# Optimization experiments

Hardware: AMD Instinct MI355X
Metric: run time of the kernel (lower is better)

The kernel has to match this reference:

```python
import jax, jax.numpy as jnp
import numpy as np

SEG_LENS = (2048, 4096, 8192)
DIL_RATES = (1, 2, 4)
DIM = 1024
HEADS = 16
HEAD_DIM = DIM // HEADS
BATCH = 1
SEQ = sum(SEG_LENS)


def _hilbert_perm(L):
    """Permutation ordering the first L row-major cells of a 2^k x 2^k grid by Hilbert distance."""
    n = 1
    while n * n < L:
        n *= 2
    idx = np.arange(n * n, dtype=np.int64)
    x = idx % n
    y = idx // n
    d = np.zeros(n * n, dtype=np.int64)
    s = n // 2
    while s > 0:
        rx = ((x & s) > 0).astype(np.int64)
        ry = ((y & s) > 0).astype(np.int64)
        d += s * s * ((3 * rx) ^ ry)
        swap = ry == 0
        flip = swap & (rx == 1)
        x = np.where(flip, s - 1 - x, x)
        y = np.where(flip, s - 1 - y, y)
        x, y = np.where(swap, y, x), np.where(swap, x, y)
        s //= 2
    return np.argsort(d[:L], kind='stable')


def _segment_attn(x_seg, wqkv, bqkv, wo, bo, rate, use_hilbert=True):
    """HilbertAttentionCore: hilbert reorder -> QKV -> dilated attention -> out proj -> inverse reorder.
    x_seg: [B, L, D] -> [B, L, D]
    """
    B, L, D = x_seg.shape
    hd = D // HEADS
    perm_np = _hilbert_perm(L)
    perm = jnp.asarray(perm_np)
    inv = jnp.asarray(np.argsort(perm_np))
    xh = x_seg[:, perm] if use_hilbert else x_seg
    qkv = xh @ wqkv + bqkv                      # [B, L, 3D]
    q, k, v = jnp.split(qkv, 3, axis=-1)
    q = q.reshape(B, L, HEADS, hd)
    k = k.reshape(B, L, HEADS, hd)
    v = v.reshape(B, L, HEADS, hd)
    Lr = L // rate
    offs = jnp.arange(HEADS) % rate             # per-head dilation offset
    hidx = jnp.arange(HEADS)

    def dilate(t):
        # position i = off + rate*j  <->  reshape(L//rate, rate)[j, off]
        tr = t.reshape(B, Lr, rate, HEADS, hd)
        return tr[:, :, offs, hidx, :]          # [B, Lr, H, hd]

    qd, kd, vd = dilate(q), dilate(k), dilate(v)
    scale = 1.0 / np.sqrt(hd).astype(np.float32)
    scores = jnp.einsum('bihd,bjhd->bhij', qd, kd) * scale
    probs = jax.nn.softmax(scores, axis=-1)
    od = jnp.einsum('bhij,bjhd->bihd', probs, vd)  # [B, Lr, H, hd]
    # scatter each head's dilated subsequence back; uncovered (head,pos) stay zero
    outr = jnp.zeros((B, Lr, rate, HEADS, hd), x_seg.dtype)
    outr = outr.at[:, :, offs, hidx, :].set(od)
    out = outr.reshape(B, L, HEADS * hd) @ wo + bo
    return out[:, inv] if use_hilbert else out


def setup_inputs() -> dict:
    key = jax.random.key(0)
    ks = jax.random.split(key, 16)
    inp = {
        'q': jax.random.normal(ks[0], (BATCH, SEQ, HEADS, HEAD_DIM), jnp.float32),
        'k': jax.random.normal(ks[1], (BATCH, SEQ, HEADS, HEAD_DIM), jnp.float32),
        'v': jax.random.normal(ks[2], (BATCH, SEQ, HEADS, HEAD_DIM), jnp.float32),
    }
    for i in range(3):
        inp[f'wqkv_{i}'] = jax.random.normal(ks[3 + 4 * i], (DIM, 3 * DIM), jnp.float32) * 0.02
        inp[f'bqkv_{i}'] = jnp.zeros((3 * DIM,), jnp.float32)
        inp[f'wo_{i}'] = jax.random.normal(ks[4 + 4 * i], (DIM, DIM), jnp.float32) * 0.02
        inp[f'bo_{i}'] = jnp.zeros((DIM,), jnp.float32)
    return inp


def reference(q, k, v,
              wqkv_0, bqkv_0, wo_0, bo_0,
              wqkv_1, bqkv_1, wo_1, bo_1,
              wqkv_2, bqkv_2, wo_2, bo_2):
    B, S, H, hd = q.shape
    x = q.reshape(B, S, H * hd)  # single-GPU path uses q only (as in the source)
    params = [(wqkv_0, bqkv_0, wo_0, bo_0),
              (wqkv_1, bqkv_1, wo_1, bo_1),
              (wqkv_2, bqkv_2, wo_2, bo_2)]
    outs = []
    pos = 0
    for (seg_len, rate), (wq, bq, wo, bo) in zip(zip(SEG_LENS, DIL_RATES), params):
        if pos >= S:
            break
        end = min(pos + seg_len, S)
        outs.append(_segment_attn(x[:, pos:end], wq, bq, wo, bo, rate))
        pos = end
    return jnp.concatenate(outs, axis=1).reshape(B, S, H, hd)
```

## Files before the change

kernel.cpp:

```cpp
#include <hip/hip_runtime.h>
#include <stdint.h>
#include <stddef.h>

typedef unsigned short u16;
typedef short bf16x8 __attribute__((ext_vector_type(8)));
typedef float f32x4 __attribute__((ext_vector_type(4)));
typedef float f32x16 __attribute__((ext_vector_type(16)));
typedef unsigned short ushort8v __attribute__((ext_vector_type(8)));
typedef int i32x2 __attribute__((ext_vector_type(2)));

#define LR 2048
#define LOG2E 1.44269504088896f

__device__ __forceinline__ u16 f2bf(float f) {
  unsigned u = __float_as_uint(f);
  unsigned r = u + 0x7fffu + ((u >> 16) & 1u);
  return (u16)(r >> 16);
}

__device__ __forceinline__ unsigned packbf(float lo, float hi) {
  return (unsigned)f2bf(lo) | ((unsigned)f2bf(hi) << 16);
}

__device__ __forceinline__ void plswap(unsigned& a, unsigned& b) {
#if __has_builtin(__builtin_amdgcn_permlane32_swap)
  i32x2 r = __builtin_amdgcn_permlane32_swap((int)a, (int)b, false, false);
  a = (unsigned)r[0];
  b = (unsigned)r[1];
#else
  asm volatile("s_nop 1\n\tv_permlane32_swap_b32 %0, %1\n\ts_nop 1"
               : "+v"(a), "+v"(b));
#endif
}
__device__ __forceinline__ float xhalf_max(float x) {
  unsigned a = __float_as_uint(x), b = __float_as_uint(x);
  plswap(a, b);
  return fmaxf(__uint_as_float(a), __uint_as_float(b));
}
__device__ __forceinline__ float xhalf_sum(float x) {
  unsigned a = __float_as_uint(x), b = __float_as_uint(x);
  plswap(a, b);
  return __uint_as_float(a) + __uint_as_float(b);
}

__device__ __forceinline__ void gl_lds16(const void* g, void* l) {
  __builtin_amdgcn_global_load_lds((__attribute__((address_space(1))) void*)g,
                                   (__attribute__((address_space(3))) void*)l,
                                   16, 0, 0);
}

__global__ void hilbert_kernel(int* __restrict__ perm) {
  int idx = blockIdx.x * 256 + threadIdx.x;
  if (idx >= 14336) return;
  int seg = (idx < 2048) ? 0 : (idx < 6144 ? 1 : 2);
  int segpos = (seg == 0) ? 0 : (seg == 1 ? 2048 : 6144);
  int L = 2048 << seg;
  int n = (seg == 2) ? 128 : 64;
  int t = idx - segpos;
  int d = (L == n * n) ? t : ((t < (L >> 1)) ? t : t + L);
  int x = 0, y = 0;
  for (int s = 1; s < n; s <<= 1) {
    int rx = 1 & (d >> 1);
    int ry = 1 & (d ^ rx);
    if (ry == 0) {
      if (rx == 1) { x = s - 1 - x; y = s - 1 - y; }
      int tmp = x; x = y; y = tmp;
    }
    x += s * rx; y += s * ry;
    d >>= 2;
  }
  perm[idx] = y * n + x;
}

__global__ void wtrans_kernel(const float* __restrict__ s0, const float* __restrict__ s1,
                              const float* __restrict__ s2, u16* __restrict__ dst,
                              int K, int N, int do_remap) {
  const int seg = blockIdx.z;
  const float* S = (seg == 0) ? s0 : (seg == 1 ? s1 : s2);
  u16* D = dst + (size_t)seg * K * N;
  __shared__ float tl[32][33];
  int n0 = blockIdx.x * 32, k0 = blockIdx.y * 32;
  int tx = threadIdx.x, ty = threadIdx.y;
  #pragma unroll
  for (int i = 0; i < 4; i++)
    tl[ty + 8 * i][tx] = S[(size_t)(k0 + ty + 8 * i) * N + n0 + tx];
  __syncthreads();
  int kk = k0 + tx;
  if (do_remap) {
    int rate = 1 << seg;
    int h = kk >> 6;
    int h2 = (h & (rate - 1)) * (16 >> seg) + (h >> seg);
    kk = h2 * 64 + (kk & 63);
  }
  #pragma unroll
  for (int i = 0; i < 4; i++)
    D[(size_t)(n0 + ty + 8 * i) * K + kk] = f2bf(tl[tx][ty + 8 * i]);
}

__global__ void gather_kernel(const float* __restrict__ x, const int* __restrict__ perm,
                              u16* __restrict__ xh) {
  int rr = blockIdx.x;
  int seg = (rr < 2048) ? 0 : (rr < 6144 ? 1 : 2);
  int segpos = (seg == 0) ? 0 : (seg == 1 ? 2048 : 6144);
  int rate = 1 << seg;
  int rl = rr - segpos;
  int t = (rl & (LR - 1)) * rate + (rl >> 11);
  int orig = segpos + perm[segpos + t];
  float4 v = *((const float4*)(x + (size_t)orig * 1024) + threadIdx.x);
  ushort4 o;
  o.x = f2bf(v.x); o.y = f2bf(v.y); o.z = f2bf(v.z); o.w = f2bf(v.w);
  *((ushort4*)(xh + (size_t)rr * 1024) + threadIdx.x) = o;
}

__global__ __launch_bounds__(256) void qkv_gemm_kernel(
    const u16* __restrict__ A, const u16* __restrict__ Bt,
    const float* __restrict__ b0, const float* __restrict__ b1,
    const float* __restrict__ b2, u16* __restrict__ C) {
  __shared__ char smem[35328];
  char* As = smem;
  char* Bs = smem + 16384;
  const int tid = threadIdx.x;
  const int lane = tid & 63, wid = tid >> 6;
  const int wm = wid >> 1, wn = wid & 1;
  const int rb = blockIdx.x, nb = blockIdx.y;
  const int seg = (rb < 16) ? 0 : (rb < 48 ? 1 : 2);
  const float* bias = (seg == 0) ? b0 : (seg == 1 ? b1 : b2);
  const size_t arow0 = (size_t)rb * 128;
  const char* Ab = (const char*)(A + arow0 * 1024);
  const char* Bb = (const char*)(Bt + ((size_t)seg * 3072 + (size_t)nb * 128) * 1024);

  f32x4 acc[4][4] = {};

  for (int kt = 0; kt < 16; kt++) {
    #pragma unroll
    for (int it = 0; it < 4; it++) {
      int p = (it * 256 + tid) * 16;
      int e = p ^ (((p >> 7) & 7) << 4);
      int row = e >> 7, col = e & 127;
      gl_lds16(Ab + (size_t)row * 2048 + kt * 128 + col, As + it * 4096 + wid * 1024);
      gl_lds16(Bb + (size_t)row * 2048 + kt * 128 + col, Bs + it * 4096 + wid * 1024);
    }
    __syncthreads();
    #pragma unroll
    for (int kc = 0; kc < 2; kc++) {
      bf16x8 af[4], bfr[4];
      #pragma unroll
      for (int m = 0; m < 4; m++) {
        int row = wm * 64 + m * 16 + (lane & 15);
        int e = row * 128 + kc * 64 + ((lane >> 4) << 4);
        af[m] = *(const bf16x8*)(As + (e ^ ((row & 7) << 4)));
      }
      #pragma unroll
      for (int n = 0; n < 4; n++) {
        int row = wn * 64 + n * 16 + (lane & 15);
        int e = row * 128 + kc * 64 + ((lane >> 4) << 4);
        bfr[n] = *(const bf16x8*)(Bs + (e ^ ((row & 7) << 4)));
      }
      #pragma unroll
      for (int m = 0; m < 4; m++)
        #pragma unroll
        for (int n = 0; n < 4; n++)
          acc[m][n] = __builtin_amdgcn_mfma_f32_16x16x32_bf16(af[m], bfr[n], acc[m][n], 0, 0, 0);
    }
    __syncthreads();
  }
  float bv[4];
  #pragma unroll
  for (int n = 0; n < 4; n++) bv[n] = bias[nb * 128 + wn * 64 + n * 16 + (lane & 15)];
  #pragma unroll
  for (int m = 0; m < 4; m++)
    #pragma unroll
    for (int n = 0; n < 4; n++)
      #pragma unroll
      for (int j = 0; j < 4; j++) {
        int r = wm * 64 + m * 16 + ((lane >> 4) << 2) + j;
        int c = wn * 64 + n * 16 + (lane & 15);
        *(u16*)(smem + r * 272 + c * 2) = f2bf(acc[m][n][j] + bv[n]);
      }
  __syncthreads();
  #pragma unroll
  for (int it = 0; it < 8; it++) {
    int ci = it * 256 + tid;
    int row = ci >> 4, c16 = ci & 15;
    bf16x8 vv = *(const bf16x8*)(smem + row * 272 + c16 * 16);
    u16* crow = C + (arow0 + row) * 3072 + nb * 128;
    *(bf16x8*)((char*)crow + c16 * 16) = vv;
  }
}

__global__ __launch_bounds__(256) void attn_kernel(const u16* __restrict__ qkv,
                                                   u16* __restrict__ opre) {
  __shared__ char smem[32768];
  const int tid = threadIdx.x;
  const int lane = tid & 63;
  const int wid = tid >> 6;
  const int l31 = lane & 31;
  const int hi = lane >> 5;
  const int by = blockIdx.y;
  const int seg = by >> 4, h = by & 15;
  const int segrow = (seg == 0) ? 0 : (seg == 1 ? 2048 : 6144);
  const int rate = 1 << seg;
  const int off = h & (rate - 1);
  const int base = segrow + off * LR;
  const int h_col = off * (16 >> seg) + (h >> seg);
  const int q0 = blockIdx.x * 128;
  const int qw = q0 + wid * 32;
  const char* qb = (const char*)qkv;

  const int vkey0 = 2 * (tid & 31);
  const int vd0 = (tid >> 5) * 8;

  #pragma unroll
  for (int it = 0; it < 2; it++) {
    int p = (it * 256 + tid) * 16;
    int e = p ^ (((p >> 7) & 7) << 4);
    int row = e >> 7, col = e & 127;
    gl_lds16(qb + (size_t)(base + row) * 6144 + 2048 + h * 128 + col,
             smem + it * 4096 + wid * 1024);
  }
  ushort8v v0r = *(const ushort8v*)(qb + (size_t)(base + vkey0) * 6144 + 4096 + h * 128 + vd0 * 2);
  ushort8v v1r = *(const ushort8v*)(qb + (size_t)(base + vkey0 + 1) * 6144 + 4096 + h * 128 + vd0 * 2);
  bf16x8 qf[4];
  #pragma unroll
  for (int i = 0; i < 4; i++)
    qf[i] = *(const bf16x8*)(qb + (size_t)(base + qw + l31) * 6144 + h * 128 + i * 32 + hi * 16);
  #pragma unroll
  for (int dd = 0; dd < 8; dd++) {
    int d = vd0 + dd;
    unsigned val = (unsigned)(u16)v0r[dd] | ((unsigned)(u16)v1r[dd] << 16);
    int addr = d * 128 + vkey0 * 2;
    *(unsigned*)(smem + 16384 + (addr ^ ((d & 7) << 4))) = val;
  }
  __syncthreads();

  float Mrun = -INFINITY, Lrun = 0.f;
  f32x16 accO0 = {}, accO1 = {};
  const float K1 = 0.125f * LOG2E;

  for (int kt = 0; kt < 32; kt++) {
    const int cur = kt & 1;
    const int nxt = cur ^ 1;
    char* Ks  = smem + (cur << 13);
    char* Vt  = smem + 16384 + (cur << 13);
    char* Ksn = smem + (nxt << 13);
    char* Vtn = smem + 16384 + (nxt << 13);
    ushort8v nv0, nv1;
    if (kt < 31) {
      #pragma unroll
      for (int it = 0; it < 2; it++) {
        int p = (it * 256 + tid) * 16;
        int e = p ^ (((p >> 7) & 7) << 4);
        int row = e >> 7, col = e & 127;
        gl_lds16(qb + (size_t)(base + (kt + 1) * 64 + row) * 6144 + 2048 + h * 128 + col,
                 Ksn + it * 4096 + wid * 1024);
      }
      nv0 = *(const ushort8v*)(qb + (size_t)(base + (kt + 1) * 64 + vkey0) * 6144 + 4096 + h * 128 + vd0 * 2);
      nv1 = *(const ushort8v*)(qb + (size_t)(base + (kt + 1) * 64 + vkey0 + 1) * 6144 + 4096 + h * 128 + vd0 * 2);
    }
    #pragma unroll
    for (int s = 0; s < 2; s++) {
      f32x16 sacc = {};
      #pragma unroll
      for (int i = 0; i < 4; i++) {
        int row = s * 32 + l31;
        int addr = (row * 128 + i * 32 + hi * 16) ^ ((row & 7) << 4);
        bf16x8 kf = *(const bf16x8*)(Ks + addr);
        sacc = __builtin_amdgcn_mfma_f32_32x32x16_bf16(kf, qf[i], sacc, 0, 0, 0);
      }
      float t8[8];
      #pragma unroll
      for (int t = 0; t < 8; t++) t8[t] = fmaxf(sacc[2 * t], sacc[2 * t + 1]);
      float m01 = fmaxf(fmaxf(t8[0], t8[1]), fmaxf(t8[2], t8[3]));
      float m23 = fmaxf(fmaxf(t8[4], t8[5]), fmaxf(t8[6], t8[7]));
      float m = xhalf_max(fmaxf(m01, m23)) * 0.125f;
      if (!__all(m - Mrun <= 8.0f)) {
        float mnew = fmaxf(Mrun, m);
        float rf = exp2f((Mrun - mnew) * LOG2E);
        Lrun *= rf;
        #pragma unroll
        for (int r = 0; r < 16; r++) { accO0[r] *= rf; accO1[r] *= rf; }
        Mrun = mnew;
      }
      float c2 = Mrun * LOG2E;
      #pragma unroll
      for (int r = 0; r < 16; r++) sacc[r] = exp2f(sacc[r] * K1 - c2);
      float s8[8];
      #pragma unroll
      for (int t = 0; t < 8; t++) s8[t] = sacc[2 * t] + sacc[2 * t + 1];
      float sm = (((s8[0] + s8[1]) + (s8[2] + s8[3])) + ((s8[4] + s8[5]) + (s8[6] + s8[7])));
      Lrun += xhalf_sum(sm);
      unsigned w[8];
      #pragma unroll
      for (int t = 0; t < 8; t++) w[t] = packbf(sacc[2 * t], sacc[2 * t + 1]);
      plswap(w[0], w[2]); plswap(w[1], w[3]);
      plswap(w[4], w[6]); plswap(w[5], w[7]);
      union PU { unsigned u[4]; bf16x8 v; };
      PU pu0, pu1;
      pu0.u[0] = w[0]; pu0.u[1] = w[1]; pu0.u[2] = w[2]; pu0.u[3] = w[3];
      pu1.u[0] = w[4]; pu1.u[1] = w[5]; pu1.u[2] = w[6]; pu1.u[3] = w[7];
      #pragma unroll
      for (int j = 0; j < 2; j++) {
        bf16x8 pa = (j == 0) ? pu0.v : pu1.v;
        #pragma unroll
        for (int dt = 0; dt < 2; dt++) {
          int d = dt * 32 + l31;
          int addr = (d * 128 + s * 64 + j * 32 + hi * 16) ^ ((d & 7) << 4);
          bf16x8 vf = *(const bf16x8*)(Vt + addr);
          if (dt == 0) accO0 = __builtin_amdgcn_mfma_f32_32x32x16_bf16(pa, vf, accO0, 0, 0, 0);
          else         accO1 = __builtin_amdgcn_mfma_f32_32x32x16_bf16(pa, vf, accO1, 0, 0, 0);
        }
      }
    }
    if (kt < 31) {
      #pragma unroll
      for (int dd = 0; dd < 8; dd++) {
        int d = vd0 + dd;
        unsigned val = (unsigned)(u16)nv0[dd] | ((unsigned)(u16)nv1[dd] << 16);
        int addr = d * 128 + vkey0 * 2;
        *(unsigned*)(Vtn + (addr ^ ((d & 7) << 4))) = val;
      }
    }
    __syncthreads();
  }

  float invL = 1.0f / Lrun;
  #pragma unroll
  for (int r = 0; r < 16; r++) {
    int qrow = (r & 3) + 8 * (r >> 2) + 4 * hi;
    float li = __shfl(invL, qrow);
    int qloc = wid * 32 + qrow;
    int a0 = (qloc * 128 + l31 * 2) ^ ((qrow & 7) << 4);
    int a1 = (qloc * 128 + 64 + l31 * 2) ^ ((qrow & 7) << 4);
    *(u16*)(smem + a0) = f2bf(accO0[r] * li);
    *(u16*)(smem + a1) = f2bf(accO1[r] * li);
  }
  __syncthreads();
  #pragma unroll
  for (int it = 0; it < 4; it++) {
    int idx = it * 256 + tid;
    int row = idx >> 3, c16 = idx & 7;
    int a = (row * 128 + c16 * 16) ^ ((row & 7) << 4);
    bf16x8 vv = *(const bf16x8*)(smem + a);
    *(bf16x8*)((char*)(opre + (size_t)(base + q0 + row) * 1024 + h_col * 64) + c16 * 16) = vv;
  }
}

__global__ __launch_bounds__(256) void out_gemm_kernel(
    const u16* __restrict__ A, const u16* __restrict__ Bt,
    const float* __restrict__ b0, const float* __restrict__ b1,
    const float* __restrict__ b2, const int* __restrict__ perm,
    float* __restrict__ Out) {
  __shared__ char smem[32768];
  __shared__ int drow[128];
  char* As = smem;
  char* Bs = smem + 16384;
  const int tid = threadIdx.x;
  const int lane = tid & 63, wid = tid >> 6;
  const int wm = wid >> 1, wn = wid & 1;
  const int rb = blockIdx.x, nb = blockIdx.y;
  const int seg = (rb < 16) ? 0 : (rb < 48 ? 1 : 2);
  const int segpos = (seg == 0) ? 0 : (seg == 1 ? 2048 : 6144);
  const int rate = 1 << seg;
  const float* bias = (seg == 0) ? b0 : (seg == 1 ? b1 : b2);
  const size_t arow0 = (size_t)rb * 128;
  const char* Ab = (const char*)(A + arow0 * 1024);
  const char* Bb = (const char*)(Bt + ((size_t)seg * 1024 + (size_t)nb * 128) * 1024);

  const int blk = (int)(arow0 - segpos) >> 11;
  const int ktpb = 16 >> seg;
  const int kt0 = blk * ktpb;

  f32x4 acc[4][4] = {};

  for (int kt = kt0; kt < kt0 + ktpb; kt++) {
    #pragma unroll
    for (int it = 0; it < 4; it++) {
      int p = (it * 256 + tid) * 16;
      int e = p ^ (((p >> 7) & 7) << 4);
      int row = e >> 7, col = e & 127;
      gl_lds16(Ab + (size_t)row * 2048 + kt * 128 + col, As + it * 4096 + wid * 1024);
      gl_lds16(Bb + (size_t)row * 2048 + kt * 128 + col, Bs + it * 4096 + wid * 1024);
    }
    __syncthreads();
    #pragma unroll
    for (int kc = 0; kc < 2; kc++) {
      bf16x8 af[4], bfr[4];
      #pragma unroll
      for (int m = 0; m < 4; m++) {
        int row = wm * 64 + m * 16 + (lane & 15);
        int e = row * 128 + kc * 64 + ((lane >> 4) << 4);
        af[m] = *(const bf16x8*)(As + (e ^ ((row & 7) << 4)));
      }
      #pragma unroll
      for (int n = 0; n < 4; n++) {
        int row = wn * 64 + n * 16 + (lane & 15);
        int e = row * 128 + kc * 64 + ((lane >> 4) << 4);
        bfr[n] = *(const bf16x8*)(Bs + (e ^ ((row & 7) << 4)));
      }
      #pragma unroll
      for (int m = 0; m < 4; m++)
        #pragma unroll
        for (int n = 0; n < 4; n++)
          acc[m][n] = __builtin_amdgcn_mfma_f32_16x16x32_bf16(af[m], bfr[n], acc[m][n], 0, 0, 0);
    }
    __syncthreads();
  }
  if (tid < 128) {
    int rl = (int)arow0 + tid - segpos;
    int t = (rl & (LR - 1)) * rate + (rl >> 11);
    drow[tid] = segpos + perm[segpos + t];
  }
  __syncthreads();
  float bv[4];
  #pragma unroll
  for (int n = 0; n < 4; n++) bv[n] = bias[nb * 128 + wn * 64 + n * 16 + (lane & 15)];
  #pragma unroll
  for (int m = 0; m < 4; m++)
    #pragma unroll
    for (int j = 0; j < 4; j++) {
      int r = wm * 64 + m * 16 + ((lane >> 4) << 2) + j;
      int gr = drow[r];
      float* orow = Out + (size_t)gr * 1024 + nb * 128 + wn * 64;
      #pragma unroll
      for (int n = 0; n < 4; n++)
        orow[n * 16 + (lane & 15)] = acc[m][n][j] + bv[n];
    }
}

extern "C" void kernel_launch(void* const* d_in, const int* in_sizes, int n_in,
                              void* d_out, int out_size, void* d_ws, size_t ws_size,
                              hipStream_t stream) {
  (void)in_sizes; (void)n_in; (void)out_size;
  const float* x = (const float*)d_in[0];
  const float* wqkv0 = (const float*)d_in[3];
  const float* bqkv0 = (const float*)d_in[4];
  const float* wo0 = (const float*)d_in[5];
  const float* bo0 = (const float*)d_in[6];
  const float* wqkv1 = (const float*)d_in[7];
  const float* bqkv1 = (const float*)d_in[8];
  const float* wo1 = (const float*)d_in[9];
  const float* bo1 = (const float*)d_in[10];
  const float* wqkv2 = (const float*)d_in[11];
  const float* bqkv2 = (const float*)d_in[12];
  const float* wo2 = (const float*)d_in[13];
  const float* bo2 = (const float*)d_in[14];

  if (ws_size < 172032000ull) return;
  char* ws = (char*)d_ws;
  int* perm = (int*)ws;
  u16* xh    = (u16*)(ws + 65536);
  u16* wqkvt = (u16*)(ws + 29425664);
  u16* wot   = (u16*)(ws + 48300032);
  u16* qkv   = (u16*)(ws + 54591488);
  u16* opre  = (u16*)(ws + 142671872);
  float* out = (float*)d_out;

  hilbert_kernel<<<56, 256, 0, stream>>>(perm);
  wtrans_kernel<<<dim3(96, 32, 3), dim3(32, 8), 0, stream>>>(wqkv0, wqkv1, wqkv2, wqkvt, 1024, 3072, 0);
  wtrans_kernel<<<dim3(32, 32, 3), dim3(32, 8), 0, stream>>>(wo0, wo1, wo2, wot, 1024, 1024, 1);
  gather_kernel<<<14336, 256, 0, stream>>>(x, perm, xh);
  qkv_gemm_kernel<<<dim3(112, 24), 256, 0, stream>>>(xh, wqkvt, bqkv0, bqkv1, bqkv2, qkv);
  attn_kernel<<<dim3(16, 48), 256, 0, stream>>>(qkv, opre);
  out_gemm_kernel<<<dim3(112, 8), 256, 0, stream>>>(opre, wot, bo0, bo1, bo2, perm, out);
}
```

Baseline: 305.7 us.

## Double-buffer LDS tiles in both GEMMs and remap QKV blocks across XCDs

Both GEMM kernels now prefetch the next K-tile into a second LDS buffer while MFMAs run on the current one, which removes one barrier per iteration and overlaps global loads with compute. The QKV GEMM also switches to a 1D grid with a block-id remap that groups consecutive tiles onto the same XCD, aiming for better L2 reuse. LDS use grows to 64KB per block, which may reduce occupancy. The epilogue reuses the start of smem for staging, and the final barrier after the loop keeps that safe.

After: 304.3 us. No clear change (-0.5%).

```diff
diff --git a/kernel.cpp b/kernel.cpp
--- a/kernel.cpp
+++ b/kernel.cpp
@@ -116,13 +116,13 @@
     const u16* __restrict__ A, const u16* __restrict__ Bt,
     const float* __restrict__ b0, const float* __restrict__ b1,
     const float* __restrict__ b2, u16* __restrict__ C) {
-  __shared__ char smem[35328];
-  char* As = smem;
-  char* Bs = smem + 16384;
+  __shared__ char smem[65536];
   const int tid = threadIdx.x;
   const int lane = tid & 63, wid = tid >> 6;
   const int wm = wid >> 1, wn = wid & 1;
-  const int rb = blockIdx.x, nb = blockIdx.y;
+  const int bid = blockIdx.x;
+  const int wg = (bid & 7) * 336 + (bid >> 3);
+  const int rb = wg / 24, nb = wg % 24;
   const int seg = (rb < 16) ? 0 : (rb < 48 ? 1 : 2);
   const float* bias = (seg == 0) ? b0 : (seg == 1 ? b1 : b2);
   const size_t arow0 = (size_t)rb * 128;
@@ -131,16 +131,32 @@
 
   f32x4 acc[4][4] = {};
 
+  #pragma unroll
+  for (int it = 0; it < 4; it++) {
+    int p = (it * 256 + tid) * 16;
+    int e = p ^ (((p >> 7) & 7) << 4);
+    int row = e >> 7, col = e & 127;
+    gl_lds16(Ab + (size_t)row * 2048 + col, smem + it * 4096 + wid * 1024);
+    gl_lds16(Bb + (size_t)row * 2048 + col, smem + 32768 + it * 4096 + wid * 1024);
+  }
+  __syncthreads();
+
   for (int kt = 0; kt < 16; kt++) {
-    #pragma unroll
-    for (int it = 0; it < 4; it++) {
-      int p = (it * 256 + tid) * 16;
-      int e = p ^ (((p >> 7) & 7) << 4);
-      int row = e >> 7, col = e & 127;
-      gl_lds16(Ab + (size_t)row * 2048 + kt * 128 + col, As + it * 4096 + wid * 1024);
-      gl_lds16(Bb + (size_t)row * 2048 + kt * 128 + col, Bs + it * 4096 + wid * 1024);
-    }
-    __syncthreads();
+    const int buf = kt & 1, nbuf = buf ^ 1;
+    char* As = smem + buf * 16384;
+    char* Bs = smem + 32768 + buf * 16384;
+    if (kt < 15) {
+      #pragma unroll
+      for (int it = 0; it < 4; it++) {
+        int p = (it * 256 + tid) * 16;
+        int e = p ^ (((p >> 7) & 7) << 4);
+        int row = e >> 7, col = e & 127;
+        gl_lds16(Ab + (size_t)row * 2048 + (kt + 1) * 128 + col,
+                 smem + nbuf * 16384 + it * 4096 + wid * 1024);
+        gl_lds16(Bb + (size_t)row * 2048 + (kt + 1) * 128 + col,
+                 smem + 32768 + nbuf * 16384 + it * 4096 + wid * 1024);
+      }
+    }
     #pragma unroll
     for (int kc = 0; kc < 2; kc++) {
       bf16x8 af[4], bfr[4];
@@ -164,6 +180,7 @@
     }
     __syncthreads();
   }
+
   float bv[4];
   #pragma unroll
   for (int n = 0; n < 4; n++) bv[n] = bias[nb * 128 + wn * 64 + n * 16 + (lane & 15)];
@@ -350,10 +367,8 @@
     const float* __restrict__ b0, const float* __restrict__ b1,
     const float* __restrict__ b2, const int* __restrict__ perm,
     float* __restrict__ Out) {
-  __shared__ char smem[32768];
+  __shared__ char smem[65536];
   __shared__ int drow[128];
-  char* As = smem;
-  char* Bs = smem + 16384;
   const int tid = threadIdx.x;
   const int lane = tid & 63, wid = tid >> 6;
   const int wm = wid >> 1, wn = wid & 1;
@@ -372,16 +387,33 @@
 
   f32x4 acc[4][4] = {};
 
-  for (int kt = kt0; kt < kt0 + ktpb; kt++) {
-    #pragma unroll
-    for (int it = 0; it < 4; it++) {
-      int p = (it * 256 + tid) * 16;
-      int e = p ^ (((p >> 7) & 7) << 4);
-      int row = e >> 7, col = e & 127;
-      gl_lds16(Ab + (size_t)row * 2048 + kt * 128 + col, As + it * 4096 + wid * 1024);
-      gl_lds16(Bb + (size_t)row * 2048 + kt * 128 + col, Bs + it * 4096 + wid * 1024);
-    }
-    __syncthreads();
+  #pragma unroll
+  for (int it = 0; it < 4; it++) {
+    int p = (it * 256 + tid) * 16;
+    int e = p ^ (((p >> 7) & 7) << 4);
+    int row = e >> 7, col = e & 127;
+    gl_lds16(Ab + (size_t)row * 2048 + kt0 * 128 + col, smem + it * 4096 + wid * 1024);
+    gl_lds16(Bb + (size_t)row * 2048 + kt0 * 128 + col, smem + 32768 + it * 4096 + wid * 1024);
+  }
+  __syncthreads();
+
+  for (int i = 0; i < ktpb; i++) {
+    const int kt = kt0 + i;
+    const int buf = i & 1, nbuf = buf ^ 1;
+    char* As = smem + buf * 16384;
+    char* Bs = smem + 32768 + buf * 16384;
+    if (i < ktpb - 1) {
+      #pragma unroll
+      for (int it = 0; it < 4; it++) {
+        int p = (it * 256 + tid) * 16;
+        int e = p ^ (((p >> 7) & 7) << 4);
+        int row = e >> 7, col = e & 127;
+        gl_lds16(Ab + (size_t)row * 2048 + (kt + 1) * 128 + col,
+                 smem + nbuf * 16384 + it * 4096 + wid * 1024);
+        gl_lds16(Bb + (size_t)row * 2048 + (kt + 1) * 128 + col,
+                 smem + 32768 + nbuf * 16384 + it * 4096 + wid * 1024);
+      }
+    }
     #pragma unroll
     for (int kc = 0; kc < 2; kc++) {
       bf16x8 af[4], bfr[4];
@@ -459,7 +491,7 @@
   wtrans_kernel<<<dim3(96, 32, 3), dim3(32, 8), 0, stream>>>(wqkv0, wqkv1, wqkv2, wqkvt, 1024, 3072, 0);
   wtrans_kernel<<<dim3(32, 32, 3), dim3(32, 8), 0, stream>>>(wo0, wo1, wo2, wot, 1024, 1024, 1);
   gather_kernel<<<14336, 256, 0, stream>>>(x, perm, xh);
-  qkv_gemm_kernel<<<dim3(112, 24), 256, 0, stream>>>(xh, wqkvt, bqkv0, bqkv1, bqkv2, qkv);
+  qkv_gemm_kernel<<<2688, 256, 0, stream>>>(xh, wqkvt, bqkv0, bqkv1, bqkv2, qkv);
   attn_kernel<<<dim3(16, 48), 256, 0, stream>>>(qkv, opre);
   out_gemm_kernel<<<dim3(112, 8), 256, 0, stream>>>(opre, wot, bo0, bo1, bo2, perm, out);
 }
```
